# Performance work log

Measured on AMD Instinct MI355X. Metric: run time of the kernel, lower is better.

## Reference

```python
import jax, jax.numpy as jnp
import numpy as np

N_HEAD = 9
HEAD_DIM = 64
KV_PER_HEAD = 21  # 189 // 9
ROPE_BASE = 10000.0


def _rotate_half(x):
    # matches torch: x1 = first half (floor), x2 = rest; cat(-x2, x1)
    h = x.shape[-1] // 2
    return jnp.concatenate([-x[..., h:], x[..., :h]], axis=-1)


def _rope_cos_sin(T, dtype):
    inv_freq = 1.0 / (ROPE_BASE ** (jnp.arange(0, KV_PER_HEAD, 2, dtype=jnp.float32) / KV_PER_HEAD))  # [11]
    t = jnp.arange(T, dtype=jnp.float32)
    freqs = jnp.einsum('i,j->ij', t, inv_freq)          # [T, 11]
    emb = jnp.concatenate([freqs, freqs], axis=-1)      # [T, 22]
    cos = jnp.cos(emb)[:, :KV_PER_HEAD].astype(dtype)   # [T, 21]
    sin = jnp.sin(emb)[:, :KV_PER_HEAD].astype(dtype)
    return cos, sin


def setup_inputs() -> dict:
    key = jax.random.key(0)
    ks = jax.random.split(key, 5)
    B, T, C = 4, 2048, 576
    kv_dim = 189
    s = 0.02
    return {
        'x': jax.random.normal(ks[0], (B, T, C), dtype=jnp.float32),
        'Wq': jax.random.normal(ks[1], (C, C), dtype=jnp.float32) * s,
        'Wk': jax.random.normal(ks[2], (C, kv_dim), dtype=jnp.float32) * s,
        'Wv': jax.random.normal(ks[3], (C, kv_dim), dtype=jnp.float32) * s,
        'Wo': jax.random.normal(ks[4], (C, C), dtype=jnp.float32) * s,
    }


def reference(x, Wq, Wk, Wv, Wo):
    B, T, C = x.shape
    q = (x @ Wq).reshape(B, T, N_HEAD, HEAD_DIM).transpose(0, 2, 1, 3)      # [B,H,T,64]
    k = (x @ Wk).reshape(B, T, N_HEAD, KV_PER_HEAD).transpose(0, 2, 1, 3)   # [B,H,T,21]
    v = (x @ Wv).reshape(B, T, N_HEAD, KV_PER_HEAD).transpose(0, 2, 1, 3)   # [B,H,T,21]

    cos, sin = _rope_cos_sin(T, x.dtype)  # [T,21] each, broadcasts over B,H
    k_rot = k * cos + _rotate_half(k) * sin
    q_part = q[..., :KV_PER_HEAD]
    q_rot_part = q_part * cos + _rotate_half(q_part) * sin
    # q dims >= KV_PER_HEAD never touch nonzero K, so only the first 21 dims matter
    scale = 1.0 / np.sqrt(HEAD_DIM)
    scores = jnp.einsum('bhqd,bhkd->bhqk', q_rot_part, k_rot) * scale       # [B,H,T,T]
    causal = jnp.tril(jnp.ones((T, T), dtype=bool))
    scores = jnp.where(causal, scores, -1e9)
    attn = jax.nn.softmax(scores, axis=-1)
    y_small = jnp.einsum('bhqk,bhkd->bhqd', attn, v)                        # [B,H,T,21]
    # zero-pad up to head_dim (matches k_pad/v_pad construction)
    y = jnp.pad(y_small, ((0, 0), (0, 0), (0, 0), (0, HEAD_DIM - KV_PER_HEAD)))
    y = y.transpose(0, 2, 1, 3).reshape(B, T, C)
    return y @ Wo
```

## Files before the change

### kernel.cpp

```cpp
#include <hip/hip_runtime.h>
#include <hip/hip_bf16.h>

typedef unsigned short u16;
typedef unsigned int u32;
typedef __attribute__((ext_vector_type(8))) short bf16x8;
typedef __attribute__((ext_vector_type(4))) float f32x4;
typedef __attribute__((ext_vector_type(4))) int i32x4;

#define N_HEADS 9
#define T_SEQ 2048
#define BATCH 4
#define CDIM 576
#define ROWS (BATCH * T_SEQ)
#define NBH (BATCH * N_HEADS)
#define PART_SLOT ((size_t)NBH * T_SEQ * 32)

__device__ __forceinline__ u16 f2bf(float f) {
    u32 u = __float_as_uint(f);
    u32 r = u + 0x7FFFu + ((u >> 16) & 1u);
    return (u16)(r >> 16);
}
__device__ __forceinline__ float bf2f(u16 u) { return __uint_as_float(((u32)u) << 16); }
__device__ __forceinline__ u32 cvt_pk_bf16(float lo, float hi) {
    u32 r;
    asm("v_cvt_pk_bf16_f32 %0, %1, %2" : "=v"(r) : "v"(lo), "v"(hi));
    return r;
}
__device__ __forceinline__ float exp2_raw(float x) {
    float r;
    asm("v_exp_f32 %0, %1" : "=v"(r) : "v"(x));
    return r;
}

__global__ __launch_bounds__(256) void prep_wt(const float* __restrict__ Wq, const float* __restrict__ Wk,
                                               const float* __restrict__ Wv, const float* __restrict__ Wo,
                                               u16* __restrict__ WcT, u16* __restrict__ WoSubT,
                                               float* __restrict__ cosT, float* __restrict__ sinT) {
    int idx = blockIdx.x * 256 + threadIdx.x;
    if (idx < 576 * 576) {
        int n = idx / 576, k = idx - n * 576;
        float v;
        if (n < 189)      v = Wq[(size_t)k * 576 + (n / 21) * 64 + (n % 21)];
        else if (n < 378) v = Wk[(size_t)k * 189 + (n - 189)];
        else if (n < 567) v = Wv[(size_t)k * 189 + (n - 378)];
        else              v = 0.f;
        WcT[(size_t)n * 576 + k] = f2bf(v);
    }
    if (idx < 576 * 192) {
        int n = idx / 192, k = idx - n * 192;
        float v = 0.f;
        if (k < 189) v = Wo[(size_t)((k / 21) * 64 + (k % 21)) * 576 + n];
        WoSubT[(size_t)n * 192 + k] = f2bf(v);
    }
    if (idx < T_SEQ * 21) {
        int t = idx / 21, d = idx - t * 21;
        int i = (d < 11) ? d : d - 11;
        float e = (2.0f * (float)i) / 21.0f;
        float invf = exp2f(-e * 13.287712379549449f);
        float ang = (float)t * invf;
        cosT[idx] = cosf(ang);
        sinT[idx] = sinf(ang);
    }
}


template <int AF32, int OUTF32>
__global__ __launch_bounds__(256) void gemm_mfma(const void* __restrict__ Av, const u16* __restrict__ BT,
                                                 void* __restrict__ Cout, int K, int lda, int ldbt, int ldc) {
    __shared__ u16 As[128][32];
    __shared__ u16 Bs[64][32];
    const int tid = threadIdx.x;
    const int lane = tid & 63, w = tid >> 6;
    const int m0 = (blockIdx.x & 63) * 128, n0 = (blockIdx.x >> 6) * 64;
    const int k15 = lane & 15, g = lane >> 4;

    const int arow = tid >> 1;
    const int ac0 = (tid & 1) * 2;
    const int brow = tid >> 2, bc = tid & 3;

    f32x4 zero = {0.f, 0.f, 0.f, 0.f};
    f32x4 acc[2][4];
#pragma unroll
    for (int hf = 0; hf < 2; hf++)
#pragma unroll
        for (int n = 0; n < 4; n++) acc[hf][n] = zero;

    const float* Af = (const float*)Av;
    const u16*   Ab = (const u16*)Av;

    float4 af0, af1, af2, af3;
    i32x4 av0, av1;
    if (AF32) {
        const float* ap = &Af[(size_t)(m0 + arow) * lda + ac0 * 8];
        af0 = *(const float4*)&ap[0];
        af1 = *(const float4*)&ap[4];
        af2 = *(const float4*)&ap[8];
        af3 = *(const float4*)&ap[12];
    } else {
        av0 = *(const i32x4*)&Ab[(size_t)(m0 + arow) * lda + ac0 * 8];
        av1 = *(const i32x4*)&Ab[(size_t)(m0 + arow) * lda + (ac0 + 1) * 8];
    }
    i32x4 bv = *(const i32x4*)&BT[(size_t)(n0 + brow) * ldbt + bc * 8];

    for (int k0 = 0; k0 < K; k0 += 32) {
        __syncthreads();
        if (AF32) {
            i32x4 w0, w1;
            w0[0] = (int)cvt_pk_bf16(af0.x, af0.y); w0[1] = (int)cvt_pk_bf16(af0.z, af0.w);
            w0[2] = (int)cvt_pk_bf16(af1.x, af1.y); w0[3] = (int)cvt_pk_bf16(af1.z, af1.w);
            w1[0] = (int)cvt_pk_bf16(af2.x, af2.y); w1[1] = (int)cvt_pk_bf16(af2.z, af2.w);
            w1[2] = (int)cvt_pk_bf16(af3.x, af3.y); w1[3] = (int)cvt_pk_bf16(af3.z, af3.w);
            *(i32x4*)&As[arow][(ac0 ^ (arow & 3)) * 8] = w0;
            *(i32x4*)&As[arow][((ac0 + 1) ^ (arow & 3)) * 8] = w1;
        } else {
            *(i32x4*)&As[arow][(ac0 ^ (arow & 3)) * 8] = av0;
            *(i32x4*)&As[arow][((ac0 + 1) ^ (arow & 3)) * 8] = av1;
        }
        *(i32x4*)&Bs[brow][(bc ^ (brow & 3)) * 8] = bv;
        __syncthreads();
        int k1 = k0 + 32;
        if (k1 < K) {
            if (AF32) {
                const float* ap = &Af[(size_t)(m0 + arow) * lda + k1 + ac0 * 8];
                af0 = *(const float4*)&ap[0];
                af1 = *(const float4*)&ap[4];
                af2 = *(const float4*)&ap[8];
                af3 = *(const float4*)&ap[12];
            } else {
                av0 = *(const i32x4*)&Ab[(size_t)(m0 + arow) * lda + k1 + ac0 * 8];
                av1 = *(const i32x4*)&Ab[(size_t)(m0 + arow) * lda + k1 + (ac0 + 1) * 8];
            }
            bv = *(const i32x4*)&BT[(size_t)(n0 + brow) * ldbt + k1 + bc * 8];
        }
        const int ar0 = w * 32 + k15;
        bf16x8 a0 = *(const bf16x8*)&As[ar0][(g ^ (ar0 & 3)) * 8];
        bf16x8 a1 = *(const bf16x8*)&As[ar0 + 16][(g ^ (ar0 & 3)) * 8];
#pragma unroll
        for (int n = 0; n < 4; n++) {
            int br = n * 16 + k15;
            bf16x8 b = *(const bf16x8*)&Bs[br][(g ^ (br & 3)) * 8];
            acc[0][n] = __builtin_amdgcn_mfma_f32_16x16x32_bf16(a0, b, acc[0][n], 0, 0, 0);
            acc[1][n] = __builtin_amdgcn_mfma_f32_16x16x32_bf16(a1, b, acc[1][n], 0, 0, 0);
        }
    }
#pragma unroll
    for (int hf = 0; hf < 2; hf++)
#pragma unroll
        for (int n = 0; n < 4; n++)
#pragma unroll
            for (int i = 0; i < 4; i++) {
                int row = m0 + w * 32 + hf * 16 + g * 4 + i;
                int col = n0 + n * 16 + k15;
                float v = acc[hf][n][i];
                if (OUTF32) ((float*)Cout)[(size_t)row * ldc + col] = v;
                else        ((u16*)Cout)[(size_t)row * ldc + col] = f2bf(v);
            }
}


__global__ __launch_bounds__(256) void repack_qkv(const u16* __restrict__ qkv,
                                                  const float* __restrict__ cosT,
                                                  const float* __restrict__ sinT,
                                                  u16* __restrict__ Qp, u16* __restrict__ Kp,
                                                  u16* __restrict__ Vp) {
    __shared__ u16 Qs[64][40];
    __shared__ u16 Ksh[64][40];
    __shared__ u16 Vsh[64][40];
    const int tid = threadIdx.x;
    const int bh = blockIdx.y;
    const int b = bh / N_HEADS, h = bh - b * N_HEADS;
    const int t0 = blockIdx.x * 64;

    const int qa = (h * 21) & ~7,        qoff = h * 21 - qa;
    const int ka = (189 + h * 21) & ~7,  koff = 189 + h * 21 - ka;
    const int va = (378 + h * 21) & ~7,  voff = 378 + h * 21 - va;

#pragma unroll
    for (int it = 0; it < 3; ++it) {
        int idx = tid + it * 256;
        int row = idx / 12;
        int r12 = idx - row * 12;
        int stream = r12 >> 2, chunk = r12 & 3;
        int off = (stream == 0) ? qa : (stream == 1) ? ka : va;
        const u16* src = qkv + (size_t)(b * T_SEQ + t0 + row) * CDIM + off + chunk * 8;
        i32x4 v = *(const i32x4*)src;
        u16* dst = (stream == 0) ? &Qs[row][0] : (stream == 1) ? &Ksh[row][0] : &Vsh[row][0];
        *(i32x4*)&dst[chunk * 8] = v;
    }
    __syncthreads();

    const int r = tid >> 2, c = tid & 3;
    const int t = t0 + r;
    const float* cr = cosT + t * 21;
    const float* sr = sinT + t * 21;
    u32 wq[4] = {0, 0, 0, 0}, wk[4] = {0, 0, 0, 0};
    const float sc = 0.18033688011112042f;
#pragma unroll
    for (int j = 0; j < 8; j++) {
        int d = c * 8 + j;
        float vq = 0.f, vk = 0.f;
        if (d < 21) {
            int pd = (d < 11) ? d + 10 : d - 11;
            float cc = cr[d], ss = sr[d];
            float qv = bf2f(Qs[r][qoff + d]),  qp = bf2f(Qs[r][qoff + pd]);
            float kv = bf2f(Ksh[r][koff + d]), kp = bf2f(Ksh[r][koff + pd]);
            float rq = (d < 11) ? -qp : qp;
            float rk = (d < 11) ? -kp : kp;
            vq = (qv * cc + rq * ss) * sc;
            vk = kv * cc + rk * ss;
        }
        wq[j >> 1] |= (u32)f2bf(vq) << ((j & 1) * 16);
        wk[j >> 1] |= (u32)f2bf(vk) << ((j & 1) * 16);
    }
    size_t obase = ((size_t)bh * T_SEQ + t) * 32 + c * 8;
    i32x4 q4; q4[0] = (int)wq[0]; q4[1] = (int)wq[1]; q4[2] = (int)wq[2]; q4[3] = (int)wq[3];
    i32x4 k4; k4[0] = (int)wk[0]; k4[1] = (int)wk[1]; k4[2] = (int)wk[2]; k4[3] = (int)wk[3];
    *(i32x4*)&Qp[obase] = q4;
    *(i32x4*)&Kp[obase] = k4;

    const int dv = tid >> 3, tc = tid & 7;
    u32 wv[4];
#pragma unroll
    for (int j = 0; j < 4; j++) {
        u16 lo, hi;
        if (dv < 21)      { lo = Vsh[tc * 8 + j * 2][voff + dv]; hi = Vsh[tc * 8 + j * 2 + 1][voff + dv]; }
        else if (dv == 31){ lo = 0x3F80; hi = 0x3F80; }
        else              { lo = 0; hi = 0; }
        wv[j] = (u32)lo | ((u32)hi << 16);
    }
    i32x4 v4; v4[0] = (int)wv[0]; v4[1] = (int)wv[1]; v4[2] = (int)wv[2]; v4[3] = (int)wv[3];
    *(i32x4*)&Vp[((size_t)bh * 32 + dv) * T_SEQ + t0 + tc * 8] = v4;
}


__global__ __launch_bounds__(512) void attn_mfma(const u16* __restrict__ Qp,
                                                 const u16* __restrict__ Kp,
                                                 const u16* __restrict__ Vp,
                                                 u16* __restrict__ Ybuf,
                                                 u16* __restrict__ Part) {
    __shared__ u16 Ks[128][40];
    __shared__ u16 Vt[32][136];
    __shared__ u16 Pt[2][8][16][72];
    const int tid = threadIdx.x;
    const int lane = tid & 63, w = tid >> 6;
    const int bh = blockIdx.y;
    const int b = bh / N_HEADS, h = bh - b * N_HEADS;
    const int k15 = lane & 15, g = lane >> 4;

    int qt2 = 15, ci = blockIdx.x;
    for (int q = 15; q >= 0; --q) {
        int n = (q >> 2) + 1;
        if (ci < n) { qt2 = q; break; }
        ci -= n;
    }
    const int q0 = qt2 * 128;
    const int n128 = qt2 + 1;
    const int nc = (qt2 >> 2) + 1;
    const int u_begin = (ci * n128) / nc;
    const int u_end = ((ci + 1) * n128) / nc;

    const bool isK = (tid < 256);
    const int krow = (tid & 255) >> 2, kc = tid & 3;
    const int vrow = (tid & 255) >> 3, vc = tid & 7;
    const u16* Kg = Kp + (size_t)bh * 65536 + krow * 32 + kc * 8;
    const u16* Vg = Vp + (size_t)bh * 65536 + vrow * 2048 + vc * 8;

    bf16x8 qf = *(const bf16x8*)&Qp[(((size_t)bh << 11) + q0 + w * 16 + k15) * 32 + g * 8];

    f32x4 y0 = {0.f, 0.f, 0.f, 0.f}, y1 = {0.f, 0.f, 0.f, 0.f};
    const int qloc = (w & 3) * 16 + k15;
    const int kd = 2 * qt2 + (w >> 2);

    u32 off = (u32)u_begin * 4096u;
    u32 voffu = (u32)u_begin * 128u;
    i32x4 r0, r1;
    if (isK) { r0 = *(const i32x4*)&Kg[off];   r1 = *(const i32x4*)&Kg[off + 2048]; }
    else     { r0 = *(const i32x4*)&Vg[voffu]; r1 = *(const i32x4*)&Vg[voffu + 64]; }

    for (int u = u_begin; u < u_end; ++u) {
        __syncthreads();
        if (isK) {
            *(i32x4*)&Ks[krow][kc * 8] = r0;
            *(i32x4*)&Ks[krow + 64][kc * 8] = r1;
        } else {
            *(i32x4*)&Vt[vrow][vc * 8] = r0;
            *(i32x4*)&Vt[vrow][vc * 8 + 64] = r1;
        }
        if (u + 1 < u_end) {
            off += 4096u; voffu += 128u;
            if (isK) { r0 = *(const i32x4*)&Kg[off];   r1 = *(const i32x4*)&Kg[off + 2048]; }
            else     { r0 = *(const i32x4*)&Vg[voffu]; r1 = *(const i32x4*)&Vg[voffu + 64]; }
        }
        __syncthreads();

        const int kt0 = u * 2;
        const bool do0 = (kt0 <= kd);
        const bool do1 = (kt0 + 1 <= kd);

        f32x4 s0[4], s1[4];
        if (do0) {
#pragma unroll
            for (int f = 0; f < 4; f++) {
                bf16x8 kf = *(const bf16x8*)&Ks[f * 16 + k15][g * 8];
                f32x4 z = {0.f, 0.f, 0.f, 0.f};
                s0[f] = __builtin_amdgcn_mfma_f32_16x16x32_bf16(kf, qf, z, 0, 0, 0);
            }
        }
        if (do1) {
#pragma unroll
            for (int f = 0; f < 4; f++) {
                bf16x8 kf = *(const bf16x8*)&Ks[64 + f * 16 + k15][g * 8];
                f32x4 z = {0.f, 0.f, 0.f, 0.f};
                s1[f] = __builtin_amdgcn_mfma_f32_16x16x32_bf16(kf, qf, z, 0, 0, 0);
            }
        }
        if (do0 && kt0 == kd) {
#pragma unroll
            for (int f = 0; f < 4; f++)
#pragma unroll
                for (int i = 0; i < 4; i++)
                    if (f * 16 + g * 4 + i > qloc) s0[f][i] = -16384.f;
        }
        if (do1 && kt0 + 1 == kd) {
#pragma unroll
            for (int f = 0; f < 4; f++)
#pragma unroll
                for (int i = 0; i < 4; i++)
                    if (f * 16 + g * 4 + i > qloc) s1[f][i] = -16384.f;
        }

        if (do0) {
#pragma unroll
            for (int f = 0; f < 4; f++) {
                u32 lo = cvt_pk_bf16(exp2_raw(s0[f][0]), exp2_raw(s0[f][1]));
                u32 hi = cvt_pk_bf16(exp2_raw(s0[f][2]), exp2_raw(s0[f][3]));
                uint2 pk; pk.x = lo; pk.y = hi;
                *(uint2*)&Pt[0][w][k15][f * 16 + g * 4] = pk;
            }
        }
        if (do1) {
#pragma unroll
            for (int f = 0; f < 4; f++) {
                u32 lo = cvt_pk_bf16(exp2_raw(s1[f][0]), exp2_raw(s1[f][1]));
                u32 hi = cvt_pk_bf16(exp2_raw(s1[f][2]), exp2_raw(s1[f][3]));
                uint2 pk; pk.x = lo; pk.y = hi;
                *(uint2*)&Pt[1][w][k15][f * 16 + g * 4] = pk;
            }
        }
        asm volatile("" ::: "memory");

        if (do0) {
#pragma unroll
            for (int kh = 0; kh < 2; kh++) {
                bf16x8 pa = *(const bf16x8*)&Pt[0][w][k15][kh * 32 + g * 8];
                bf16x8 v0 = *(const bf16x8*)&Vt[k15][kh * 32 + g * 8];
                bf16x8 v1 = *(const bf16x8*)&Vt[16 + k15][kh * 32 + g * 8];
                y0 = __builtin_amdgcn_mfma_f32_16x16x32_bf16(pa, v0, y0, 0, 0, 0);
                y1 = __builtin_amdgcn_mfma_f32_16x16x32_bf16(pa, v1, y1, 0, 0, 0);
            }
        }
        if (do1) {
#pragma unroll
            for (int kh = 0; kh < 2; kh++) {
                bf16x8 pa = *(const bf16x8*)&Pt[1][w][k15][kh * 32 + g * 8];
                bf16x8 v0 = *(const bf16x8*)&Vt[k15][64 + kh * 32 + g * 8];
                bf16x8 v1 = *(const bf16x8*)&Vt[16 + k15][64 + kh * 32 + g * 8];
                y0 = __builtin_amdgcn_mfma_f32_16x16x32_bf16(pa, v0, y0, 0, 0, 0);
                y1 = __builtin_amdgcn_mfma_f32_16x16x32_bf16(pa, v1, y1, 0, 0, 0);
            }
        }
        asm volatile("" ::: "memory");
    }

    if (nc == 1) {
#pragma unroll
        for (int i = 0; i < 4; i++) {
            float li = __shfl(y1[i], (lane & 48) + 15);
            float inv = 1.0f / li;
            int rowY = b * T_SEQ + q0 + w * 16 + g * 4 + i;
            u16* yr = &Ybuf[(size_t)rowY * 192 + h * 21];
            yr[k15] = f2bf(y0[i] * inv);
            if (k15 < 5) yr[16 + k15] = f2bf(y1[i] * inv);
        }
    } else {
#pragma unroll
        for (int i = 0; i < 4; i++) {
            size_t pb = (size_t)ci * PART_SLOT +
                        (((size_t)bh << 11) + q0 + w * 16 + g * 4 + i) * 32;
            Part[pb + k15] = f2bf(y0[i]);
            Part[pb + 16 + k15] = f2bf(y1[i]);
        }
    }
}

__global__ __launch_bounds__(256) void attn_reduce(const u16* __restrict__ Part, u16* __restrict__ Ybuf) {
    int gid = blockIdx.x * 256 + threadIdx.x;
    int d = gid & 31;
    int rest = gid >> 5;
    int t = 512 + (rest % 1536);
    int bh = rest / 1536;
    int b = bh / N_HEADS, h = bh - b * N_HEADS;
    int nc = (t >> 9) + 1;
    size_t base = (((size_t)bh << 11) + t) * 32;
    float l = 0.f, v = 0.f;
    for (int ci = 0; ci < nc; ci++) {
        l += bf2f(Part[(size_t)ci * PART_SLOT + base + 31]);
        if (d < 21) v += bf2f(Part[(size_t)ci * PART_SLOT + base + d]);
    }
    if (d < 21) Ybuf[(size_t)(b * T_SEQ + t) * 192 + h * 21 + d] = f2bf(v / l);
}


extern "C" void kernel_launch(void* const* d_in, const int* in_sizes, int n_in,
                              void* d_out, int out_size, void* d_ws, size_t ws_size,
                              hipStream_t stream) {
    const float* x  = (const float*)d_in[0];
    const float* Wq = (const float*)d_in[1];
    const float* Wk = (const float*)d_in[2];
    const float* Wv = (const float*)d_in[3];
    const float* Wo = (const float*)d_in[4];
    float* out = (float*)d_out;

    char* p = (char*)d_ws;
    auto alloc = [&](size_t bytes) { char* r = p; p += (bytes + 255) & ~(size_t)255; return r; };
    u16*   QpKp   = (u16*)alloc((size_t)ROWS * CDIM * 2);
    u16*   qkv    = (u16*)alloc((size_t)ROWS * CDIM * 2);
    u16*   WcT    = (u16*)alloc((size_t)576 * 576 * 2);
    u16*   WoSubT = (u16*)alloc((size_t)576 * 192 * 2);
    float* cosT   = (float*)alloc((size_t)T_SEQ * 21 * 4);
    float* sinT   = (float*)alloc((size_t)T_SEQ * 21 * 4);
    u16*   Vp     = (u16*)alloc((size_t)NBH * 32 * T_SEQ * 2);
    u16*   Ybuf   = (u16*)alloc((size_t)ROWS * 192 * 2);
    u16*   Part   = (u16*)alloc((size_t)4 * PART_SLOT * 2);

    u16* Qp = QpKp;
    u16* Kp = QpKp + (size_t)NBH * T_SEQ * 32;

    prep_wt<<<dim3((576 * 576 + 255) / 256), dim3(256), 0, stream>>>(Wq, Wk, Wv, Wo, WcT, WoSubT, cosT, sinT);

    gemm_mfma<1, 0><<<dim3(64 * 9), dim3(256), 0, stream>>>((const void*)x, WcT, (void*)qkv, 576, 576, 576, 576);

    repack_qkv<<<dim3(T_SEQ / 64, NBH), dim3(256), 0, stream>>>(qkv, cosT, sinT, Qp, Kp, Vp);

    attn_mfma<<<dim3(40, NBH), dim3(512), 0, stream>>>(Qp, Kp, Vp, Ybuf, Part);
    attn_reduce<<<dim3(NBH * 1536 * 32 / 256), dim3(256), 0, stream>>>(Part, Ybuf);

    gemm_mfma<0, 1><<<dim3(64 * 9), dim3(256), 0, stream>>>((const void*)Ybuf, WoSubT, (void*)out, 192, 192, 192, 576);
}
```

Measured before the change: 77.73 us.

## Double-buffer K/V shared tiles and raise wave priority around MFMA blocks

K and V tiles in shared memory now use two buffers. The first tile is staged before the loop, and each iteration writes the next tile into the alternate buffer. This removes one __syncthreads per iteration and lets the shared-memory stores overlap with MFMA work on the current tile. The MFMA sections are also wrapped in s_setprio raises, and the do0/do1 branches are nested. The cost is double the K/V LDS footprint, which could reduce occupancy.

```diff
diff --git a/kernel.cpp b/kernel.cpp
--- a/kernel.cpp
+++ b/kernel.cpp
@@ -238,8 +238,8 @@
                                                  const u16* __restrict__ Vp,
                                                  u16* __restrict__ Ybuf,
                                                  u16* __restrict__ Part) {
-    __shared__ u16 Ks[128][40];
-    __shared__ u16 Vt[32][136];
+    __shared__ u16 Ks[2][128][40];
+    __shared__ u16 Vt[2][32][136];
     __shared__ u16 Pt[2][8][16][72];
     const int tid = threadIdx.x;
     const int lane = tid & 63, w = tid >> 6;
@@ -271,65 +271,80 @@
     const int qloc = (w & 3) * 16 + k15;
     const int kd = 2 * qt2 + (w >> 2);
 
-    u32 off = (u32)u_begin * 4096u;
+    u32 koff = (u32)u_begin * 4096u;
     u32 voffu = (u32)u_begin * 128u;
     i32x4 r0, r1;
-    if (isK) { r0 = *(const i32x4*)&Kg[off];   r1 = *(const i32x4*)&Kg[off + 2048]; }
-    else     { r0 = *(const i32x4*)&Vg[voffu]; r1 = *(const i32x4*)&Vg[voffu + 64]; }
-
+    if (isK) { r0 = *(const i32x4*)&Kg[koff];   r1 = *(const i32x4*)&Kg[koff + 2048]; }
+    else     { r0 = *(const i32x4*)&Vg[voffu];  r1 = *(const i32x4*)&Vg[voffu + 64]; }
+    if (isK) {
+        *(i32x4*)&Ks[0][krow][kc * 8] = r0;
+        *(i32x4*)&Ks[0][krow + 64][kc * 8] = r1;
+    } else {
+        *(i32x4*)&Vt[0][vrow][vc * 8] = r0;
+        *(i32x4*)&Vt[0][vrow][vc * 8 + 64] = r1;
+    }
+    if (u_begin + 1 < u_end) {
+        koff += 4096u; voffu += 128u;
+        if (isK) { r0 = *(const i32x4*)&Kg[koff];   r1 = *(const i32x4*)&Kg[koff + 2048]; }
+        else     { r0 = *(const i32x4*)&Vg[voffu];  r1 = *(const i32x4*)&Vg[voffu + 64]; }
+    }
+
+    int cur = 0;
     for (int u = u_begin; u < u_end; ++u) {
         __syncthreads();
-        if (isK) {
-            *(i32x4*)&Ks[krow][kc * 8] = r0;
-            *(i32x4*)&Ks[krow + 64][kc * 8] = r1;
-        } else {
-            *(i32x4*)&Vt[vrow][vc * 8] = r0;
-            *(i32x4*)&Vt[vrow][vc * 8 + 64] = r1;
-        }
         if (u + 1 < u_end) {
-            off += 4096u; voffu += 128u;
-            if (isK) { r0 = *(const i32x4*)&Kg[off];   r1 = *(const i32x4*)&Kg[off + 2048]; }
-            else     { r0 = *(const i32x4*)&Vg[voffu]; r1 = *(const i32x4*)&Vg[voffu + 64]; }
-        }
-        __syncthreads();
+            if (isK) {
+                *(i32x4*)&Ks[cur ^ 1][krow][kc * 8] = r0;
+                *(i32x4*)&Ks[cur ^ 1][krow + 64][kc * 8] = r1;
+            } else {
+                *(i32x4*)&Vt[cur ^ 1][vrow][vc * 8] = r0;
+                *(i32x4*)&Vt[cur ^ 1][vrow][vc * 8 + 64] = r1;
+            }
+            if (u + 2 < u_end) {
+                koff += 4096u; voffu += 128u;
+                if (isK) { r0 = *(const i32x4*)&Kg[koff];   r1 = *(const i32x4*)&Kg[koff + 2048]; }
+                else     { r0 = *(const i32x4*)&Vg[voffu];  r1 = *(const i32x4*)&Vg[voffu + 64]; }
+            }
+        }
 
         const int kt0 = u * 2;
         const bool do0 = (kt0 <= kd);
         const bool do1 = (kt0 + 1 <= kd);
 
-        f32x4 s0[4], s1[4];
         if (do0) {
+            f32x4 s0[4], s1[4];
+            __builtin_amdgcn_s_setprio(1);
 #pragma unroll
             for (int f = 0; f < 4; f++) {
-                bf16x8 kf = *(const bf16x8*)&Ks[f * 16 + k15][g * 8];
+                bf16x8 kf = *(const bf16x8*)&Ks[cur][f * 16 + k15][g * 8];
                 f32x4 z = {0.f, 0.f, 0.f, 0.f};
                 s0[f] = __builtin_amdgcn_mfma_f32_16x16x32_bf16(kf, qf, z, 0, 0, 0);
             }
-        }
-        if (do1) {
-#pragma unroll
-            for (int f = 0; f < 4; f++) {
-                bf16x8 kf = *(const bf16x8*)&Ks[64 + f * 16 + k15][g * 8];
-                f32x4 z = {0.f, 0.f, 0.f, 0.f};
-                s1[f] = __builtin_amdgcn_mfma_f32_16x16x32_bf16(kf, qf, z, 0, 0, 0);
-            }
-        }
-        if (do0 && kt0 == kd) {
-#pragma unroll
-            for (int f = 0; f < 4; f++)
-#pragma unroll
-                for (int i = 0; i < 4; i++)
-                    if (f * 16 + g * 4 + i > qloc) s0[f][i] = -16384.f;
-        }
-        if (do1 && kt0 + 1 == kd) {
-#pragma unroll
-            for (int f = 0; f < 4; f++)
-#pragma unroll
-                for (int i = 0; i < 4; i++)
-                    if (f * 16 + g * 4 + i > qloc) s1[f][i] = -16384.f;
-        }
-
-        if (do0) {
+            if (do1) {
+#pragma unroll
+                for (int f = 0; f < 4; f++) {
+                    bf16x8 kf = *(const bf16x8*)&Ks[cur][64 + f * 16 + k15][g * 8];
+                    f32x4 z = {0.f, 0.f, 0.f, 0.f};
+                    s1[f] = __builtin_amdgcn_mfma_f32_16x16x32_bf16(kf, qf, z, 0, 0, 0);
+                }
+            }
+            __builtin_amdgcn_s_setprio(0);
+
+            if (kt0 == kd) {
+#pragma unroll
+                for (int f = 0; f < 4; f++)
+#pragma unroll
+                    for (int i = 0; i < 4; i++)
+                        if (f * 16 + g * 4 + i > qloc) s0[f][i] = -16384.f;
+            }
+            if (do1 && kt0 + 1 == kd) {
+#pragma unroll
+                for (int f = 0; f < 4; f++)
+#pragma unroll
+                    for (int i = 0; i < 4; i++)
+                        if (f * 16 + g * 4 + i > qloc) s1[f][i] = -16384.f;
+            }
+
 #pragma unroll
             for (int f = 0; f < 4; f++) {
                 u32 lo = cvt_pk_bf16(exp2_raw(s0[f][0]), exp2_raw(s0[f][1]));
@@ -337,39 +352,40 @@
                 uint2 pk; pk.x = lo; pk.y = hi;
                 *(uint2*)&Pt[0][w][k15][f * 16 + g * 4] = pk;
             }
-        }
-        if (do1) {
-#pragma unroll
-            for (int f = 0; f < 4; f++) {
-                u32 lo = cvt_pk_bf16(exp2_raw(s1[f][0]), exp2_raw(s1[f][1]));
-                u32 hi = cvt_pk_bf16(exp2_raw(s1[f][2]), exp2_raw(s1[f][3]));
-                uint2 pk; pk.x = lo; pk.y = hi;
-                *(uint2*)&Pt[1][w][k15][f * 16 + g * 4] = pk;
-            }
-        }
-        asm volatile("" ::: "memory");
-
-        if (do0) {
+            if (do1) {
+#pragma unroll
+                for (int f = 0; f < 4; f++) {
+                    u32 lo = cvt_pk_bf16(exp2_raw(s1[f][0]), exp2_raw(s1[f][1]));
+                    u32 hi = cvt_pk_bf16(exp2_raw(s1[f][2]), exp2_raw(s1[f][3]));
+                    uint2 pk; pk.x = lo; pk.y = hi;
+                    *(uint2*)&Pt[1][w][k15][f * 16 + g * 4] = pk;
+                }
+            }
+            asm volatile("" ::: "memory");
+
+            __builtin_amdgcn_s_setprio(1);
 #pragma unroll
             for (int kh = 0; kh < 2; kh++) {
                 bf16x8 pa = *(const bf16x8*)&Pt[0][w][k15][kh * 32 + g * 8];
-                bf16x8 v0 = *(const bf16x8*)&Vt[k15][kh * 32 + g * 8];
-                bf16x8 v1 = *(const bf16x8*)&Vt[16 + k15][kh * 32 + g * 8];
+                bf16x8 v0 = *(const bf16x8*)&Vt[cur][k15][kh * 32 + g * 8];
+                bf16x8 v1 = *(const bf16x8*)&Vt[cur][16 + k15][kh * 32 + g * 8];
                 y0 = __builtin_amdgcn_mfma_f32_16x16x32_bf16(pa, v0, y0, 0, 0, 0);
                 y1 = __builtin_amdgcn_mfma_f32_16x16x32_bf16(pa, v1, y1, 0, 0, 0);
             }
-        }
-        if (do1) {
-#pragma unroll
-            for (int kh = 0; kh < 2; kh++) {
-                bf16x8 pa = *(const bf16x8*)&Pt[1][w][k15][kh * 32 + g * 8];
-                bf16x8 v0 = *(const bf16x8*)&Vt[k15][64 + kh * 32 + g * 8];
-                bf16x8 v1 = *(const bf16x8*)&Vt[16 + k15][64 + kh * 32 + g * 8];
-                y0 = __builtin_amdgcn_mfma_f32_16x16x32_bf16(pa, v0, y0, 0, 0, 0);
-                y1 = __builtin_amdgcn_mfma_f32_16x16x32_bf16(pa, v1, y1, 0, 0, 0);
-            }
-        }
-        asm volatile("" ::: "memory");
+            if (do1) {
+#pragma unroll
+                for (int kh = 0; kh < 2; kh++) {
+                    bf16x8 pa = *(const bf16x8*)&Pt[1][w][k15][kh * 32 + g * 8];
+                    bf16x8 v0 = *(const bf16x8*)&Vt[cur][k15][64 + kh * 32 + g * 8];
+                    bf16x8 v1 = *(const bf16x8*)&Vt[cur][16 + k15][64 + kh * 32 + g * 8];
+                    y0 = __builtin_amdgcn_mfma_f32_16x16x32_bf16(pa, v0, y0, 0, 0, 0);
+                    y1 = __builtin_amdgcn_mfma_f32_16x16x32_bf16(pa, v1, y1, 0, 0, 0);
+                }
+            }
+            __builtin_amdgcn_s_setprio(0);
+            asm volatile("" ::: "memory");
+        }
+        cur ^= 1;
     }
 
     if (nc == 1) {
```

Result: no change. 77.88 us (+0.2%).
